# Kernel tuning notes

Measured on AMD Instinct MI355X. Metric: run time of the kernel, lower is better.

Reference implementation:

```python
import jax, jax.numpy as jnp
import numpy as np

D_MODEL = 1024
NUM_HEADS = 16
D_K = D_MODEL // NUM_HEADS
D_FF = 4096
EPS = 1e-5


def setup_inputs() -> dict:
    key = jax.random.key(0)
    ks = jax.random.split(key, 16)
    B, S = 2, 2048
    s_attn = 1.0 / np.sqrt(D_MODEL)
    s_ff1 = 1.0 / np.sqrt(D_MODEL)
    s_ff2 = 1.0 / np.sqrt(D_FF)
    return {
        "x": jax.random.normal(ks[0], (B, S, D_MODEL), jnp.float32),
        "Wq": jax.random.normal(ks[1], (D_MODEL, D_MODEL), jnp.float32) * s_attn,
        "bq": jnp.zeros((D_MODEL,), jnp.float32),
        "Wk": jax.random.normal(ks[2], (D_MODEL, D_MODEL), jnp.float32) * s_attn,
        "bk": jnp.zeros((D_MODEL,), jnp.float32),
        "Wv": jax.random.normal(ks[3], (D_MODEL, D_MODEL), jnp.float32) * s_attn,
        "bv": jnp.zeros((D_MODEL,), jnp.float32),
        "Wo": jax.random.normal(ks[4], (D_MODEL, D_MODEL), jnp.float32) * s_attn,
        "bo": jnp.zeros((D_MODEL,), jnp.float32),
        "W1": jax.random.normal(ks[5], (D_MODEL, D_FF), jnp.float32) * s_ff1,
        "b1": jnp.zeros((D_FF,), jnp.float32),
        "W2": jax.random.normal(ks[6], (D_FF, D_MODEL), jnp.float32) * s_ff2,
        "b2": jnp.zeros((D_MODEL,), jnp.float32),
        "g1": jnp.ones((D_MODEL,), jnp.float32),
        "be1": jnp.zeros((D_MODEL,), jnp.float32),
        "g2": jnp.ones((D_MODEL,), jnp.float32),
        "be2": jnp.zeros((D_MODEL,), jnp.float32),
    }


def _layernorm(x, g, b):
    m = jnp.mean(x, axis=-1, keepdims=True)
    v = jnp.mean(jnp.square(x - m), axis=-1, keepdims=True)
    return (x - m) * jax.lax.rsqrt(v + EPS) * g + b


def _split_heads(x, B, S):
    # (B, S, D) -> (B, H, S, d_k)
    return x.reshape(B, S, NUM_HEADS, D_K).transpose(0, 2, 1, 3)


def reference(x, Wq, bq, Wk, bk, Wv, bv, Wo, bo, W1, b1, W2, b2, g1, be1, g2, be2):
    B, S, _ = x.shape
    Q = _split_heads(x @ Wq + bq, B, S)
    K = _split_heads(x @ Wk + bk, B, S)
    V = _split_heads(x @ Wv + bv, B, S)
    scores = jnp.einsum("bhqd,bhkd->bhqk", Q, K) / np.sqrt(D_K).astype(np.float32)
    attn = jax.nn.softmax(scores, axis=-1)  # dropout is identity (p=0 / eval)
    ctx = jnp.einsum("bhqk,bhkd->bhqd", attn, V)
    ctx = ctx.transpose(0, 2, 1, 3).reshape(B, S, D_MODEL)
    attn_out = ctx @ Wo + bo
    h = _layernorm(x + attn_out, g1, be1)
    ff = jax.nn.relu(h @ W1 + b1) @ W2 + b2
    out = _layernorm(h + ff, g2, be2)
    return out, attn
```

## Files before the change

### kernel.cpp

```cpp
#include <hip/hip_runtime.h>
#include <cstddef>
#include <cstdint>

#define D_MODEL 1024
#define NUM_HEADS 16
#define DK 64
#define D_FF 4096
#define SEQ 2048
#define BATCH 2
#define EPS 1e-5f

typedef unsigned short u16;
typedef __attribute__((ext_vector_type(8))) short bf16x8;
typedef __attribute__((ext_vector_type(8))) unsigned short us8;
typedef __attribute__((ext_vector_type(4))) unsigned short us4;
typedef __attribute__((ext_vector_type(4))) float f32x4;

#define SBAR() asm volatile("s_barrier" ::: "memory")

__device__ __forceinline__ u16 f2b(float f) {
    unsigned u = __float_as_uint(f);
    u += 0x7fffu + ((u >> 16) & 1u);
    return (u16)(u >> 16);
}
__device__ __forceinline__ float b2f(u16 v) {
    return __uint_as_float((unsigned)v << 16);
}

__device__ __forceinline__ void gload16(const void* g, void* l) {
    __builtin_amdgcn_global_load_lds(
        (const __attribute__((address_space(1))) void*)g,
        (__attribute__((address_space(3))) void*)l, 16, 0, 0);
}

__device__ __forceinline__ void stage_half(
    const u16* __restrict__ g, int ld, long kbase, int h,
    u16* dst, int tid, int wid)
{
#pragma unroll
    for (int r = 0; r < 2; ++r) {
        const int ci  = r * 512 + tid;
        const int row = ci >> 2;
        const int wd  = ci & 3;
        const int f   = (row + (row >> 2)) & 3;
        const long src = (long)row * ld + kbase + (long)(h * 4 + (wd ^ f)) * 8;
        gload16(g + src, dst + (r * 512 + wid * 64) * 8);
    }
}

__device__ __forceinline__ bf16x8 frag64(const u16* base, int ks, int row, int g) {
    const int f = (row + (row >> 2)) & 3;
    return *(const bf16x8*)&base[ks * 8192 + row * 32 + ((g ^ f) * 8)];
}

template<int KTOT, bool RELU>
__global__ __launch_bounds__(512, 2) void gemm256(
    const u16* __restrict__ Abf, const u16* __restrict__ BT,
    const float* __restrict__ bias0, u16* __restrict__ C0,
    int ldc, int nx)
{
    constexpr int NT = KTOT / 64;
    __shared__ u16 lds[2][32768];

    const int tid = threadIdx.x;
    const int wid = tid >> 6, l = tid & 63;
    const int r16 = l & 15, g = l >> 4;
    const int wr = wid >> 2, wc = wid & 3;

    const int nwg = gridDim.x;
    const int q = nwg >> 3, rr = nwg & 7;
    const int xcd = blockIdx.x & 7, idx = blockIdx.x >> 3;
    const int wg = (xcd < rr ? xcd * (q + 1) : rr * (q + 1) + (xcd - rr) * q) + idx;
    const long bm = (long)(wg / nx) * 256;
    const long bn = (long)(wg % nx) * 256;

    const u16* Ag = Abf + bm * KTOT;
    const u16* Bg = BT + bn * KTOT;

    f32x4 acc[8][4];
#pragma unroll
    for (int i = 0; i < 8; ++i)
#pragma unroll
        for (int n = 0; n < 4; ++n)
            acc[i][n] = (f32x4){0.f, 0.f, 0.f, 0.f};

    stage_half(Ag, KTOT, 0, 0, &lds[0][0],     tid, wid);
    stage_half(Ag, KTOT, 0, 1, &lds[0][8192],  tid, wid);
    stage_half(Bg, KTOT, 0, 0, &lds[0][16384], tid, wid);
    stage_half(Bg, KTOT, 0, 1, &lds[0][24576], tid, wid);
    if (NT > 1) {
        stage_half(Ag, KTOT, 64, 0, &lds[1][0],     tid, wid);
        stage_half(Bg, KTOT, 64, 0, &lds[1][16384], tid, wid);
    }
    asm volatile("s_waitcnt vmcnt(4)" ::: "memory");
    SBAR();

    for (int t = 0; t < NT; ++t) {
        u16* cur = &lds[t & 1][0];
        u16* nxt = &lds[(t + 1) & 1][0];
        const long k1 = (long)(t + 1) * 64;
        const long k2 = (long)(t + 2) * 64;
        const bool s1 = (t + 1 < NT), s2 = (t + 2 < NT);

        bf16x8 a0[4], b0[4];
#pragma unroll
        for (int i = 0; i < 4; ++i) {
            a0[i] = frag64(cur,         0, wr * 128 + i * 16 + r16, g);
            b0[i] = frag64(cur + 16384, 0, wc * 64  + i * 16 + r16, g);
        }
        if (s1) stage_half(Ag, KTOT, k1, 1, nxt + 8192, tid, wid);
        SBAR();
        __builtin_amdgcn_s_setprio(1);
#pragma unroll
        for (int i = 0; i < 4; ++i)
#pragma unroll
            for (int n = 0; n < 4; ++n)
                acc[i][n] = __builtin_amdgcn_mfma_f32_16x16x32_bf16(
                    a0[i], b0[n], acc[i][n], 0, 0, 0);
        __builtin_amdgcn_s_setprio(0);
        SBAR();

        bf16x8 a1[4];
#pragma unroll
        for (int i = 0; i < 4; ++i)
            a1[i] = frag64(cur, 0, wr * 128 + (i + 4) * 16 + r16, g);
        if (s1) stage_half(Bg, KTOT, k1, 1, nxt + 24576, tid, wid);
        SBAR();
        __builtin_amdgcn_s_setprio(1);
#pragma unroll
        for (int i = 0; i < 4; ++i)
#pragma unroll
            for (int n = 0; n < 4; ++n)
                acc[i + 4][n] = __builtin_amdgcn_mfma_f32_16x16x32_bf16(
                    a1[i], b0[n], acc[i + 4][n], 0, 0, 0);
        __builtin_amdgcn_s_setprio(0);
        SBAR();

        bf16x8 a2[4], b1[4];
#pragma unroll
        for (int i = 0; i < 4; ++i) {
            a2[i] = frag64(cur,         1, wr * 128 + i * 16 + r16, g);
            b1[i] = frag64(cur + 16384, 1, wc * 64  + i * 16 + r16, g);
        }
        if (s2) stage_half(Ag, KTOT, k2, 0, cur, tid, wid);
        SBAR();
        __builtin_amdgcn_s_setprio(1);
#pragma unroll
        for (int i = 0; i < 4; ++i)
#pragma unroll
            for (int n = 0; n < 4; ++n)
                acc[i][n] = __builtin_amdgcn_mfma_f32_16x16x32_bf16(
                    a2[i], b1[n], acc[i][n], 0, 0, 0);
        __builtin_amdgcn_s_setprio(0);
        SBAR();

        bf16x8 a3[4];
#pragma unroll
        for (int i = 0; i < 4; ++i)
            a3[i] = frag64(cur, 1, wr * 128 + (i + 4) * 16 + r16, g);
        if (s2) stage_half(Bg, KTOT, k2, 0, cur + 16384, tid, wid);
        SBAR();
        __builtin_amdgcn_s_setprio(1);
#pragma unroll
        for (int i = 0; i < 4; ++i)
#pragma unroll
            for (int n = 0; n < 4; ++n)
                acc[i + 4][n] = __builtin_amdgcn_mfma_f32_16x16x32_bf16(
                    a3[i], b1[n], acc[i + 4][n], 0, 0, 0);
        __builtin_amdgcn_s_setprio(0);
        if (s2)      asm volatile("s_waitcnt vmcnt(4)" ::: "memory");
        else if (s1) asm volatile("s_waitcnt vmcnt(0)" ::: "memory");
        SBAR();
    }

    const long crow0 = bm + wr * 128 + g * 4;
    const long ccol0 = bn + wc * 64 + r16;
#pragma unroll
    for (int n = 0; n < 4; ++n) {
        const long col = ccol0 + n * 16;
        const float bv = bias0[col];
#pragma unroll
        for (int i = 0; i < 8; ++i)
#pragma unroll
            for (int j = 0; j < 4; ++j) {
                const long row = crow0 + i * 16 + j;
                float v = acc[i][n][j] + bv;
                if (RELU) v = fmaxf(v, 0.f);
                C0[row * (long)ldc + col] = f2b(v);
            }
    }
}

template<bool RELU, int NSPLIT>
__global__ __launch_bounds__(256) void gemm_mfma(
    const u16* __restrict__ Abf, const u16* __restrict__ BT,
    const float* __restrict__ bias0, const float* __restrict__ bias1,
    const float* __restrict__ bias2,
    u16* __restrict__ C0, u16* __restrict__ C1, u16* __restrict__ C2,
    int lda, int ldb, int ldc, int K, int nx)
{
    constexpr int BM = 128, BN = 128;
    constexpr int MI = 4, NI = 4;
    constexpr int RA = 2, RB = 2;
    constexpr int TILE = (BM + BN) * 32;

    __shared__ u16 sm[2][TILE];

    const int tid = threadIdx.x;
    const int w = tid >> 6, l = tid & 63;
    const int r16 = l & 15, g = l >> 4;
    const int wr = w >> 1, wc = w & 1;

    const int nwg = gridDim.x;
    const int q = nwg >> 3, rr = nwg & 7;
    const int xcd = blockIdx.x & 7, idx = blockIdx.x >> 3;
    const int wg = (xcd < rr ? xcd * (q + 1) : rr * (q + 1) + (xcd - rr) * q) + idx;
    const long bm = (long)(wg / nx) * BM;
    const long bn = (long)(wg % nx) * BN;

    f32x4 acc[MI][NI];
#pragma unroll
    for (int mi = 0; mi < MI; ++mi)
#pragma unroll
        for (int ni = 0; ni < NI; ++ni)
            acc[mi][ni] = (f32x4){0.f, 0.f, 0.f, 0.f};

    long aOff[RA], bOff[RB];
#pragma unroll
    for (int r = 0; r < RA; ++r) {
        int c = r * 256 + tid;
        aOff[r] = (long)(bm + (c >> 2)) * lda + (c & 3) * 8;
    }
#pragma unroll
    for (int r = 0; r < RB; ++r) {
        int c = r * 256 + tid;
        bOff[r] = (long)(bn + (c >> 2)) * ldb + (c & 3) * 8;
    }

#pragma unroll
    for (int r = 0; r < RA; ++r)
        gload16(Abf + aOff[r], &sm[0][0] + (r * 256 + w * 64) * 8);
#pragma unroll
    for (int r = 0; r < RB; ++r)
        gload16(BT + bOff[r], &sm[0][BM * 32] + (r * 256 + w * 64) * 8);
    __syncthreads();

    int cur = 0;
    for (int k0 = 0; k0 < K; k0 += 32) {
        if (k0 + 32 < K) {
            const int nxt = cur ^ 1;
#pragma unroll
            for (int r = 0; r < RA; ++r)
                gload16(Abf + aOff[r] + k0 + 32, &sm[nxt][0] + (r * 256 + w * 64) * 8);
#pragma unroll
            for (int r = 0; r < RB; ++r)
                gload16(BT + bOff[r] + k0 + 32, &sm[nxt][BM * 32] + (r * 256 + w * 64) * 8);
        }

        const u16* smA = &sm[cur][0];
        const u16* smB = &sm[cur][BM * 32];
        bf16x8 af[MI], bfr[NI];
#pragma unroll
        for (int mi = 0; mi < MI; ++mi)
            af[mi] = *(const bf16x8*)&smA[(wr * 64 + mi * 16 + r16) * 32 + g * 8];
#pragma unroll
        for (int ni = 0; ni < NI; ++ni)
            bfr[ni] = *(const bf16x8*)&smB[(wc * 64 + ni * 16 + r16) * 32 + g * 8];
#pragma unroll
        for (int mi = 0; mi < MI; ++mi)
#pragma unroll
            for (int ni = 0; ni < NI; ++ni)
                acc[mi][ni] = __builtin_amdgcn_mfma_f32_16x16x32_bf16(
                    af[mi], bfr[ni], acc[mi][ni], 0, 0, 0);

        __syncthreads();
        cur ^= 1;
    }

    u16* Cb = C0; const float* bp = bias0; long coff = 0;
    if (NSPLIT == 3) {
        const int grp = (int)(bn >> 10);
        if (grp == 1)      { Cb = C1; bp = bias1; }
        else if (grp == 2) { Cb = C2; bp = bias2; }
        coff = (long)grp << 10;
    }
    const long crow0 = bm + wr * 64 + g * 4;
    const long ccol0 = bn + wc * 64 + r16 - coff;
#pragma unroll
    for (int ni = 0; ni < NI; ++ni) {
        const long col = ccol0 + ni * 16;
        const float bv = bp[col];
#pragma unroll
        for (int mi = 0; mi < MI; ++mi) {
#pragma unroll
            for (int j = 0; j < 4; ++j) {
                const long row = crow0 + mi * 16 + j;
                float v = acc[mi][ni][j] + bv;
                if (RELU) v = fmaxf(v, 0.f);
                Cb[row * (long)ldc + col] = f2b(v);
            }
        }
    }
}

#define QBLK 128
#define KBLK 64
#define NTT (SEQ / KBLK)
#define C2E 0.18033688f

__global__ __launch_bounds__(256) void flash_attn(
    const u16* __restrict__ Qg, const u16* __restrict__ Kg,
    const u16* __restrict__ Vt, float* __restrict__ attn,
    u16* __restrict__ ctx)
{
    __shared__ u16 smem[16384];
    __shared__ u16 Ps[4][2048];
    __shared__ float stats[4][32];

    u16* const Qs  = smem;
    u16* const kb0 = smem + 8192;
    u16* const kb1 = smem;

    const int tid = threadIdx.x;
    const int w = tid >> 6, l = tid & 63;
    const int r16 = l & 15, g = l >> 4;

    const int wg = (blockIdx.x & 7) * (gridDim.x >> 3) + (blockIdx.x >> 3);
    const int qb = wg & 15, z = wg >> 4;
    const int b = z >> 4, h = z & 15;
    const long q0 = (long)qb * QBLK;

    const long kBase = ((long)b * SEQ) * D_MODEL + h * DK;
    const long vBase = (long)z * DK * SEQ;

#pragma unroll
    for (int r = 0; r < 4; ++r) {
        int c = r * 256 + tid;
        int row = c >> 3, bl = c & 7;
        long src = ((long)b * SEQ + q0 + row) * D_MODEL + h * DK
                 + ((bl ^ (row & 7)) * 8);
        gload16(Qg + src, Qs + (r * 256 + w * 64) * 8);
    }
#pragma unroll
    for (int r = 0; r < 2; ++r) {
        int c = r * 256 + tid;
        int row = c >> 3, bl = c & 7;
        gload16(Kg + kBase + (long)row * D_MODEL + ((bl ^ (row & 7)) * 8),
                kb0 + (r * 256 + w * 64) * 8);
    }
    __syncthreads();

    bf16x8 qf[2][2];
#pragma unroll
    for (int qi = 0; qi < 2; ++qi)
#pragma unroll
        for (int ks = 0; ks < 2; ++ks)
            qf[qi][ks] = *(const bf16x8*)
                &Qs[(w * 32 + qi * 16 + r16) * 64 + (((ks * 4 + g) ^ (r16 & 7)) * 8)];
    __syncthreads();

    float lrun[2] = {0.f, 0.f};

    for (int t = 0; t < NTT; ++t) {
        if (t + 1 < NTT) {
            u16* kdst = ((t + 1) & 1) ? kb1 : kb0;
            const long kro = (long)(t + 1) * KBLK;
#pragma unroll
            for (int r = 0; r < 2; ++r) {
                int c = r * 256 + tid;
                int row = c >> 3, bl = c & 7;
                gload16(Kg + kBase + (kro + row) * D_MODEL + ((bl ^ (row & 7)) * 8),
                        kdst + (r * 256 + w * 64) * 8);
            }
        }
        const u16* kcur = (t & 1) ? kb1 : kb0;

        f32x4 sT[4][2];
#pragma unroll
        for (int ki = 0; ki < 4; ++ki)
#pragma unroll
            for (int qi = 0; qi < 2; ++qi) sT[ki][qi] = (f32x4){0.f, 0.f, 0.f, 0.f};

        __builtin_amdgcn_s_setprio(1);
#pragma unroll
        for (int ks = 0; ks < 2; ++ks) {
            bf16x8 kf[4];
#pragma unroll
            for (int ki = 0; ki < 4; ++ki)
                kf[ki] = *(const bf16x8*)
                    &kcur[(ki * 16 + r16) * 64 + (((ks * 4 + g) ^ (r16 & 7)) * 8)];
#pragma unroll
            for (int ki = 0; ki < 4; ++ki)
#pragma unroll
                for (int qi = 0; qi < 2; ++qi)
                    sT[ki][qi] = __builtin_amdgcn_mfma_f32_16x16x32_bf16(
                        kf[ki], qf[qi][ks], sT[ki][qi], 0, 0, 0);
        }
        __builtin_amdgcn_s_setprio(0);

#pragma unroll
        for (int qi = 0; qi < 2; ++qi) {
            float ls = 0.f;
#pragma unroll
            for (int ki = 0; ki < 4; ++ki)
#pragma unroll
                for (int j = 0; j < 4; ++j)
                    ls += exp2f(sT[ki][qi][j] * C2E);
            ls += __shfl_xor(ls, 16);
            ls += __shfl_xor(ls, 32);
            lrun[qi] += ls;
        }
        __syncthreads();
    }

    u16* const p2b0 = smem + 8192;
    u16* const p2b1 = smem;
#pragma unroll
    for (int r = 0; r < 2; ++r) {
        int c = r * 256 + tid;
        int row = c >> 3, bl = c & 7;
        gload16(Kg + kBase + (long)row * D_MODEL + ((bl ^ (row & 7)) * 8),
                p2b0 + (r * 256 + w * 64) * 8);
        gload16(Vt + vBase + (long)row * SEQ + ((bl ^ (row & 7)) * 8),
                p2b0 + 4096 + (r * 256 + w * 64) * 8);
    }
    if (l < 16) {
        stats[w][r16]      = 1.0f / lrun[0];
        stats[w][16 + r16] = 1.0f / lrun[1];
    }
    __syncthreads();

    float il2[2][4];
#pragma unroll
    for (int mi = 0; mi < 2; ++mi)
#pragma unroll
        for (int j = 0; j < 4; ++j)
            il2[mi][j] = stats[w][mi * 16 + g * 4 + j];

    f32x4 acc2[2][4];
#pragma unroll
    for (int mi = 0; mi < 2; ++mi)
#pragma unroll
        for (int ni = 0; ni < 4; ++ni) acc2[mi][ni] = (f32x4){0.f, 0.f, 0.f, 0.f};

    for (int t = 0; t < NTT; ++t) {
        const int k0 = t * KBLK;
        if (t + 1 < NTT) {
            u16* dst = ((t + 1) & 1) ? p2b1 : p2b0;
            const long kro = (long)(t + 1) * KBLK;
#pragma unroll
            for (int r = 0; r < 2; ++r) {
                int c = r * 256 + tid;
                int row = c >> 3, bl = c & 7;
                gload16(Kg + kBase + (kro + row) * D_MODEL + ((bl ^ (row & 7)) * 8),
                        dst + (r * 256 + w * 64) * 8);
                gload16(Vt + vBase + (long)row * SEQ + kro + ((bl ^ (row & 7)) * 8),
                        dst + 4096 + (r * 256 + w * 64) * 8);
            }
        }
        const u16* kcur = (t & 1) ? p2b1 : p2b0;
        const u16* vcur = kcur + 4096;

        f32x4 s[2][4];
#pragma unroll
        for (int mi = 0; mi < 2; ++mi)
#pragma unroll
            for (int ni = 0; ni < 4; ++ni) s[mi][ni] = (f32x4){0.f, 0.f, 0.f, 0.f};

        __builtin_amdgcn_s_setprio(1);
#pragma unroll
        for (int ks = 0; ks < 2; ++ks) {
            bf16x8 kf[4];
#pragma unroll
            for (int ni = 0; ni < 4; ++ni)
                kf[ni] = *(const bf16x8*)
                    &kcur[(ni * 16 + r16) * 64 + (((ks * 4 + g) ^ (r16 & 7)) * 8)];
#pragma unroll
            for (int mi = 0; mi < 2; ++mi)
#pragma unroll
                for (int ni = 0; ni < 4; ++ni)
                    s[mi][ni] = __builtin_amdgcn_mfma_f32_16x16x32_bf16(
                        qf[mi][ks], kf[ni], s[mi][ni], 0, 0, 0);
        }
        __builtin_amdgcn_s_setprio(0);

#pragma unroll
        for (int mi = 0; mi < 2; ++mi)
#pragma unroll
            for (int j = 0; j < 4; ++j) {
                const int pr = mi * 16 + g * 4 + j;
                const long grow = (long)z * SEQ + q0 + w * 32 + pr;
#pragma unroll
                for (int ni = 0; ni < 4; ++ni) {
                    float p = exp2f(s[mi][ni][j] * C2E) * il2[mi][j];
                    const int pc = ni * 16 + r16;
                    __builtin_nontemporal_store(p, &attn[grow * SEQ + k0 + pc]);
                    Ps[w][pr * 64 + (pc ^ ((pr & 7) << 3))] = f2b(p);
                }
            }

        __builtin_amdgcn_s_setprio(1);
#pragma unroll
        for (int ks = 0; ks < 2; ++ks) {
            bf16x8 pf[2], vf[4];
#pragma unroll
            for (int mi = 0; mi < 2; ++mi)
                pf[mi] = *(const bf16x8*)
                    &Ps[w][(mi * 16 + r16) * 64 + (((ks * 4 + g) ^ (r16 & 7)) * 8)];
#pragma unroll
            for (int ni = 0; ni < 4; ++ni)
                vf[ni] = *(const bf16x8*)
                    &vcur[(ni * 16 + r16) * 64 + (((ks * 4 + g) ^ (r16 & 7)) * 8)];
#pragma unroll
            for (int mi = 0; mi < 2; ++mi)
#pragma unroll
                for (int ni = 0; ni < 4; ++ni)
                    acc2[mi][ni] = __builtin_amdgcn_mfma_f32_16x16x32_bf16(
                        pf[mi], vf[ni], acc2[mi][ni], 0, 0, 0);
        }
        __builtin_amdgcn_s_setprio(0);
        __syncthreads();
    }

#pragma unroll
    for (int mi = 0; mi < 2; ++mi)
#pragma unroll
        for (int j = 0; j < 4; ++j) {
            const long grow = (long)b * SEQ + q0 + w * 32 + mi * 16 + g * 4 + j;
#pragma unroll
            for (int ni = 0; ni < 4; ++ni)
                ctx[grow * D_MODEL + h * DK + ni * 16 + r16] = f2b(acc2[mi][ni][j]);
        }
}

__device__ __forceinline__ void tr32(
    const float* __restrict__ W, u16* __restrict__ Wt, int R, int C,
    int bx, int by, int tx, int ty, float (*t)[33])
{
    const long c = (long)bx * 32 + tx;
    const long r0 = (long)by * 32;
#pragma unroll
    for (int j = 0; j < 32; j += 8)
        t[ty + j][tx] = W[(r0 + ty + j) * C + c];
    __syncthreads();
    const long r = r0 + tx;
#pragma unroll
    for (int j = 0; j < 32; j += 8)
        Wt[((long)bx * 32 + ty + j) * R + r] = f2b(t[tx][ty + j]);
}

__global__ __launch_bounds__(256) void preproc(
    const float* __restrict__ x, u16* __restrict__ x_bf,
    const float* __restrict__ Wq, const float* __restrict__ Wk,
    const float* __restrict__ Wv, const float* __restrict__ Wo,
    u16* __restrict__ Wqkvo_t,
    const float* __restrict__ W1, u16* __restrict__ W1t,
    const float* __restrict__ W2, u16* __restrict__ W2t)
{
    __shared__ float t[32][33];
    int bid = blockIdx.x;
    const int tx = threadIdx.x & 31, ty = threadIdx.x >> 5;

    if (bid < 2048) {
        long i = ((long)bid * 256 + threadIdx.x) * 8;
        float4 a = *(const float4*)(x + i);
        float4 b = *(const float4*)(x + i + 4);
        us8 o;
        o[0] = f2b(a.x); o[1] = f2b(a.y); o[2] = f2b(a.z); o[3] = f2b(a.w);
        o[4] = f2b(b.x); o[5] = f2b(b.y); o[6] = f2b(b.z); o[7] = f2b(b.w);
        *(us8*)(x_bf + i) = o;
        return;
    }
    bid -= 2048;
    if (bid < 4096) {
        const int z = bid >> 10, rem = bid & 1023;
        const float* W = (z == 0) ? Wq : (z == 1) ? Wk : (z == 2) ? Wv : Wo;
        tr32(W, Wqkvo_t + (size_t)z * D_MODEL * D_MODEL, D_MODEL, D_MODEL,
             rem & 31, rem >> 5, tx, ty, t);
        return;
    }
    bid -= 4096;
    if (bid < 4096) {
        tr32(W1, W1t, D_MODEL, D_FF, bid & 127, bid >> 7, tx, ty, t);
        return;
    }
    bid -= 4096;
    {
        tr32(W2, W2t, D_FF, D_MODEL, bid & 31, bid >> 5, tx, ty, t);
    }
}

__global__ __launch_bounds__(256) void transpose_v(
    const u16* __restrict__ V, u16* __restrict__ Vt)
{
    __shared__ u16 t[32][33];
    const int z = blockIdx.z, b = z >> 4, h = z & 15;
    const int tx = threadIdx.x & 31, ty = threadIdx.x >> 5;
    const long k0 = (long)blockIdx.x * 32;
    const long d0 = (long)blockIdx.y * 32;
#pragma unroll
    for (int j = 0; j < 32; j += 8)
        t[ty + j][tx] = V[((long)b * SEQ + k0 + ty + j) * D_MODEL + h * DK + d0 + tx];
    __syncthreads();
#pragma unroll
    for (int j = 0; j < 32; j += 8)
        Vt[((long)z * DK + d0 + ty + j) * SEQ + k0 + tx] = t[tx][ty + j];
}

template<int OM>
__global__ __launch_bounds__(256) void add_ln_kernel(
    const u16* __restrict__ a, const u16* __restrict__ b,
    const float* __restrict__ g, const float* __restrict__ be,
    void* __restrict__ outp)
{
    const int l = threadIdx.x & 63, w = threadIdx.x >> 6;
    const long row = (long)blockIdx.x * 4 + w;
    const long base = row * D_MODEL;

    float xv[16];
#pragma unroll
    for (int c = 0; c < 2; ++c) {
        const long off = c * 512 + l * 8;
        us8 av = *(const us8*)(a + base + off);
        us8 bv = *(const us8*)(b + base + off);
#pragma unroll
        for (int i = 0; i < 8; ++i)
            xv[c * 8 + i] = b2f(av[i]) + b2f(bv[i]);
    }

    float s = 0.f;
#pragma unroll
    for (int i = 0; i < 16; ++i) s += xv[i];
#pragma unroll
    for (int off = 1; off < 64; off <<= 1) s += __shfl_xor(s, off);
    const float mean = s * (1.0f / D_MODEL);

    float ss = 0.f;
#pragma unroll
    for (int i = 0; i < 16; ++i) {
        xv[i] -= mean;
        ss += xv[i] * xv[i];
    }
#pragma unroll
    for (int off = 1; off < 64; off <<= 1) ss += __shfl_xor(ss, off);
    const float rs = rsqrtf(ss * (1.0f / D_MODEL) + EPS);

#pragma unroll
    for (int c = 0; c < 2; ++c) {
        const long off = c * 512 + l * 8;
        float4 g0 = *(const float4*)(g + off);
        float4 g1 = *(const float4*)(g + off + 4);
        float4 b0 = *(const float4*)(be + off);
        float4 b1 = *(const float4*)(be + off + 4);
        float o[8];
        o[0] = xv[c*8+0] * rs * g0.x + b0.x;
        o[1] = xv[c*8+1] * rs * g0.y + b0.y;
        o[2] = xv[c*8+2] * rs * g0.z + b0.z;
        o[3] = xv[c*8+3] * rs * g0.w + b0.w;
        o[4] = xv[c*8+4] * rs * g1.x + b1.x;
        o[5] = xv[c*8+5] * rs * g1.y + b1.y;
        o[6] = xv[c*8+6] * rs * g1.z + b1.z;
        o[7] = xv[c*8+7] * rs * g1.w + b1.w;
        if (OM == 0) {
            float4 v0 = {o[0], o[1], o[2], o[3]};
            float4 v1 = {o[4], o[5], o[6], o[7]};
            *(float4*)((float*)outp + base + off) = v0;
            *(float4*)((float*)outp + base + off + 4) = v1;
        } else {
            us8 ob;
#pragma unroll
            for (int i = 0; i < 8; ++i) ob[i] = f2b(o[i]);
            *(us8*)((u16*)outp + base + off) = ob;
        }
    }
}

extern "C" void kernel_launch(void* const* d_in, const int* in_sizes, int n_in,
                              void* d_out, int out_size, void* d_ws, size_t ws_size,
                              hipStream_t stream)
{
    const float* x   = (const float*)d_in[0];
    const float* Wq  = (const float*)d_in[1];
    const float* bq  = (const float*)d_in[2];
    const float* Wk  = (const float*)d_in[3];
    const float* bk  = (const float*)d_in[4];
    const float* Wv  = (const float*)d_in[5];
    const float* bv  = (const float*)d_in[6];
    const float* Wo  = (const float*)d_in[7];
    const float* bo  = (const float*)d_in[8];
    const float* W1  = (const float*)d_in[9];
    const float* b1  = (const float*)d_in[10];
    const float* W2  = (const float*)d_in[11];
    const float* b2  = (const float*)d_in[12];
    const float* g1  = (const float*)d_in[13];
    const float* be1 = (const float*)d_in[14];
    const float* g2  = (const float*)d_in[15];
    const float* be2 = (const float*)d_in[16];

    float* out  = (float*)d_out;
    float* attn = out + (size_t)BATCH * SEQ * D_MODEL;

    char* ws = (char*)d_ws;
    const size_t MB = 1u << 20;
    u16* x_bf    = (u16*)(ws);
    u16* Q_bf    = (u16*)(ws + 8 * MB);
    u16* K_bf    = (u16*)(ws + 16 * MB);
    u16* V_bf    = (u16*)(ws + 24 * MB);
    u16* Vt      = (u16*)(ws + 32 * MB);
    u16* Wqkvo_t = (u16*)(ws + 40 * MB);
    u16* W1t     = (u16*)(ws + 48 * MB);
    u16* W2t     = (u16*)(ws + 56 * MB);
    u16* ff1_bf  = (u16*)(ws + 64 * MB);
    u16* ctx_bf  = (u16*)(ws + 96 * MB);
    u16* Wot     = Wqkvo_t + (size_t)3 * D_MODEL * D_MODEL;
    u16* h_bf    = K_bf;
    u16* ao_bf   = V_bf;
    u16* ff2_bf  = Vt;

    const int M = BATCH * SEQ;
    dim3 T(256);

    preproc<<<dim3(2048 + 3 * 4096), T, 0, stream>>>(
        x, x_bf, Wq, Wk, Wv, Wo, Wqkvo_t, W1, W1t, W2, W2t);

    gemm_mfma<false, 3><<<dim3((M / 128) * 24), T, 0, stream>>>(
        x_bf, Wqkvo_t, bq, bk, bv, Q_bf, K_bf, V_bf,
        D_MODEL, D_MODEL, D_MODEL, D_MODEL, 24);

    transpose_v<<<dim3(SEQ / 32, DK / 32, BATCH * NUM_HEADS), T, 0, stream>>>(V_bf, Vt);

    flash_attn<<<dim3((SEQ / QBLK) * BATCH * NUM_HEADS), T, 0, stream>>>(
        Q_bf, K_bf, Vt, attn, ctx_bf);

    gemm_mfma<false, 1><<<dim3((M / 128) * 8), T, 0, stream>>>(
        ctx_bf, Wot, bo, nullptr, nullptr, ao_bf, nullptr, nullptr,
        D_MODEL, D_MODEL, D_MODEL, D_MODEL, 8);

    add_ln_kernel<1><<<dim3(M / 4), T, 0, stream>>>(x_bf, ao_bf, g1, be1, h_bf);

    gemm256<D_MODEL, true><<<dim3((M / 256) * (D_FF / 256)), dim3(512), 0, stream>>>(
        h_bf, W1t, b1, ff1_bf, D_FF, D_FF / 256);

    gemm_mfma<false, 1><<<dim3((M / 128) * 8), T, 0, stream>>>(
        ff1_bf, W2t, b2, nullptr, nullptr, ff2_bf, nullptr, nullptr,
        D_FF, D_FF, D_MODEL, D_FF, 8);

    add_ln_kernel<0><<<dim3(M / 4), T, 0, stream>>>(h_bf, ff2_bf, g2, be2, out);
}
```

Measured before the change: 409.2 us.

## Fuse V transpose into QKV GEMM epilogue and transpose scores for vector attn stores

The QKV GEMM epilogue now writes the V third directly in head-transposed layout (Vt), which removes the separate transpose_v kernel and its round trip through global memory. In the second attention pass, scores are computed as K·Q^T so each lane holds four consecutive key columns. That lets the fp32 attention probabilities go out as 16-byte nontemporal stores and the bf16 P tile be written as 8-byte LDS stores, and the per-row inverse sums now live in registers instead of a shared stats array. The V epilogue writes become 8-byte scattered stores into rows of length SEQ, which may be less coalesced than the original row-major writes.

```diff
diff --git a/kernel.cpp b/kernel.cpp
--- a/kernel.cpp
+++ b/kernel.cpp
@@ -277,14 +277,36 @@
         cur ^= 1;
     }
 
+    const long crow0 = bm + wr * 64 + g * 4;
+
+    if (NSPLIT == 3 && bn >= 2048) {
+        const int btok = (int)(crow0 >> 11);
+        const int kr0  = (int)(crow0 & 2047);
+        const long ccolV = bn + wc * 64 + r16 - 2048;
+#pragma unroll
+        for (int ni = 0; ni < NI; ++ni) {
+            const long col = ccolV + ni * 16;
+            const int h = (int)(col >> 6), d = (int)(col & 63);
+            const float bv = bias2[col];
+            const long vrow = ((long)(btok * 16 + h) * 64 + d) * (long)SEQ;
+#pragma unroll
+            for (int mi = 0; mi < MI; ++mi) {
+                us4 pv;
+#pragma unroll
+                for (int j = 0; j < 4; ++j)
+                    pv[j] = f2b(acc[mi][ni][j] + bv);
+                *(us4*)&C2[vrow + kr0 + mi * 16] = pv;
+            }
+        }
+        return;
+    }
+
     u16* Cb = C0; const float* bp = bias0; long coff = 0;
     if (NSPLIT == 3) {
         const int grp = (int)(bn >> 10);
-        if (grp == 1)      { Cb = C1; bp = bias1; }
-        else if (grp == 2) { Cb = C2; bp = bias2; }
+        if (grp == 1) { Cb = C1; bp = bias1; }
         coff = (long)grp << 10;
     }
-    const long crow0 = bm + wr * 64 + g * 4;
     const long ccol0 = bn + wc * 64 + r16 - coff;
 #pragma unroll
     for (int ni = 0; ni < NI; ++ni) {
@@ -315,7 +337,6 @@
 {
     __shared__ u16 smem[16384];
     __shared__ u16 Ps[4][2048];
-    __shared__ float stats[4][32];
 
     u16* const Qs  = smem;
     u16* const kb0 = smem + 8192;
@@ -412,6 +433,8 @@
         }
         __syncthreads();
     }
+
+    const float il[2] = {1.0f / lrun[0], 1.0f / lrun[1]};
 
     u16* const p2b0 = smem + 8192;
     u16* const p2b1 = smem;
@@ -424,24 +447,15 @@
         gload16(Vt + vBase + (long)row * SEQ + ((bl ^ (row & 7)) * 8),
                 p2b0 + 4096 + (r * 256 + w * 64) * 8);
     }
-    if (l < 16) {
-        stats[w][r16]      = 1.0f / lrun[0];
-        stats[w][16 + r16] = 1.0f / lrun[1];
-    }
     __syncthreads();
 
-    float il2[2][4];
+    f32x4 acc2[2][4];
 #pragma unroll
     for (int mi = 0; mi < 2; ++mi)
 #pragma unroll
-        for (int j = 0; j < 4; ++j)
-            il2[mi][j] = stats[w][mi * 16 + g * 4 + j];
-
-    f32x4 acc2[2][4];
-#pragma unroll
-    for (int mi = 0; mi < 2; ++mi)
-#pragma unroll
         for (int ni = 0; ni < 4; ++ni) acc2[mi][ni] = (f32x4){0.f, 0.f, 0.f, 0.f};
+
+    const long arow0 = ((long)z * SEQ + q0 + w * 32) * (long)SEQ;
 
     for (int t = 0; t < NTT; ++t) {
         const int k0 = t * KBLK;
@@ -461,43 +475,48 @@
         const u16* kcur = (t & 1) ? p2b1 : p2b0;
         const u16* vcur = kcur + 4096;
 
-        f32x4 s[2][4];
-#pragma unroll
-        for (int mi = 0; mi < 2; ++mi)
-#pragma unroll
-            for (int ni = 0; ni < 4; ++ni) s[mi][ni] = (f32x4){0.f, 0.f, 0.f, 0.f};
+        f32x4 sT[4][2];
+#pragma unroll
+        for (int ki = 0; ki < 4; ++ki)
+#pragma unroll
+            for (int qi = 0; qi < 2; ++qi) sT[ki][qi] = (f32x4){0.f, 0.f, 0.f, 0.f};
 
         __builtin_amdgcn_s_setprio(1);
 #pragma unroll
         for (int ks = 0; ks < 2; ++ks) {
             bf16x8 kf[4];
 #pragma unroll
-            for (int ni = 0; ni < 4; ++ni)
-                kf[ni] = *(const bf16x8*)
-                    &kcur[(ni * 16 + r16) * 64 + (((ks * 4 + g) ^ (r16 & 7)) * 8)];
-#pragma unroll
-            for (int mi = 0; mi < 2; ++mi)
-#pragma unroll
-                for (int ni = 0; ni < 4; ++ni)
-                    s[mi][ni] = __builtin_amdgcn_mfma_f32_16x16x32_bf16(
-                        qf[mi][ks], kf[ni], s[mi][ni], 0, 0, 0);
+            for (int ki = 0; ki < 4; ++ki)
+                kf[ki] = *(const bf16x8*)
+                    &kcur[(ki * 16 + r16) * 64 + (((ks * 4 + g) ^ (r16 & 7)) * 8)];
+#pragma unroll
+            for (int ki = 0; ki < 4; ++ki)
+#pragma unroll
+                for (int qi = 0; qi < 2; ++qi)
+                    sT[ki][qi] = __builtin_amdgcn_mfma_f32_16x16x32_bf16(
+                        kf[ki], qf[qi][ks], sT[ki][qi], 0, 0, 0);
         }
         __builtin_amdgcn_s_setprio(0);
 
 #pragma unroll
-        for (int mi = 0; mi < 2; ++mi)
-#pragma unroll
-            for (int j = 0; j < 4; ++j) {
-                const int pr = mi * 16 + g * 4 + j;
-                const long grow = (long)z * SEQ + q0 + w * 32 + pr;
-#pragma unroll
-                for (int ni = 0; ni < 4; ++ni) {
-                    float p = exp2f(s[mi][ni][j] * C2E) * il2[mi][j];
-                    const int pc = ni * 16 + r16;
-                    __builtin_nontemporal_store(p, &attn[grow * SEQ + k0 + pc]);
-                    Ps[w][pr * 64 + (pc ^ ((pr & 7) << 3))] = f2b(p);
-                }
+        for (int qi = 0; qi < 2; ++qi) {
+            const long ar = arow0 + (long)(qi * 16 + r16) * SEQ + k0 + g * 4;
+            const int prow = (qi * 16 + r16) * 64;
+#pragma unroll
+            for (int ki = 0; ki < 4; ++ki) {
+                f32x4 p;
+                p[0] = exp2f(sT[ki][qi][0] * C2E) * il[qi];
+                p[1] = exp2f(sT[ki][qi][1] * C2E) * il[qi];
+                p[2] = exp2f(sT[ki][qi][2] * C2E) * il[qi];
+                p[3] = exp2f(sT[ki][qi][3] * C2E) * il[qi];
+                __builtin_nontemporal_store(p, (f32x4*)&attn[ar + ki * 16]);
+                us4 pb;
+                pb[0] = f2b(p[0]); pb[1] = f2b(p[1]);
+                pb[2] = f2b(p[2]); pb[3] = f2b(p[3]);
+                const int kblk = 2 * ki + (g >> 1);
+                *(us4*)&Ps[w][prow + ((kblk ^ (r16 & 7)) << 3) + ((g & 1) << 2)] = pb;
             }
+        }
 
         __builtin_amdgcn_s_setprio(1);
 #pragma unroll
@@ -506,7 +525,7 @@
 #pragma unroll
             for (int mi = 0; mi < 2; ++mi)
                 pf[mi] = *(const bf16x8*)
-                    &Ps[w][(mi * 16 + r16) * 64 + (((ks * 4 + g) ^ (r16 & 7)) * 8)];
+                    &Ps[w][(mi * 16 + r16) * 64 + (((ks * 4 + g) ^ (r16 & 7)) << 3)];
 #pragma unroll
             for (int ni = 0; ni < 4; ++ni)
                 vf[ni] = *(const bf16x8*)
@@ -588,23 +607,6 @@
     {
         tr32(W2, W2t, D_FF, D_MODEL, bid & 31, bid >> 5, tx, ty, t);
     }
-}
-
-__global__ __launch_bounds__(256) void transpose_v(
-    const u16* __restrict__ V, u16* __restrict__ Vt)
-{
-    __shared__ u16 t[32][33];
-    const int z = blockIdx.z, b = z >> 4, h = z & 15;
-    const int tx = threadIdx.x & 31, ty = threadIdx.x >> 5;
-    const long k0 = (long)blockIdx.x * 32;
-    const long d0 = (long)blockIdx.y * 32;
-#pragma unroll
-    for (int j = 0; j < 32; j += 8)
-        t[ty + j][tx] = V[((long)b * SEQ + k0 + ty + j) * D_MODEL + h * DK + d0 + tx];
-    __syncthreads();
-#pragma unroll
-    for (int j = 0; j < 32; j += 8)
-        Vt[((long)z * DK + d0 + ty + j) * SEQ + k0 + tx] = t[tx][ty + j];
 }
 
 template<int OM>
@@ -705,8 +707,8 @@
     u16* x_bf    = (u16*)(ws);
     u16* Q_bf    = (u16*)(ws + 8 * MB);
     u16* K_bf    = (u16*)(ws + 16 * MB);
-    u16* V_bf    = (u16*)(ws + 24 * MB);
-    u16* Vt      = (u16*)(ws + 32 * MB);
+    u16* Vt      = (u16*)(ws + 24 * MB);
+    u16* spare   = (u16*)(ws + 32 * MB);
     u16* Wqkvo_t = (u16*)(ws + 40 * MB);
     u16* W1t     = (u16*)(ws + 48 * MB);
     u16* W2t     = (u16*)(ws + 56 * MB);
@@ -714,7 +716,7 @@
     u16* ctx_bf  = (u16*)(ws + 96 * MB);
     u16* Wot     = Wqkvo_t + (size_t)3 * D_MODEL * D_MODEL;
     u16* h_bf    = K_bf;
-    u16* ao_bf   = V_bf;
+    u16* ao_bf   = spare;
     u16* ff2_bf  = Vt;
 
     const int M = BATCH * SEQ;
@@ -724,10 +726,8 @@
         x, x_bf, Wq, Wk, Wv, Wo, Wqkvo_t, W1, W1t, W2, W2t);
 
     gemm_mfma<false, 3><<<dim3((M / 128) * 24), T, 0, stream>>>(
-        x_bf, Wqkvo_t, bq, bk, bv, Q_bf, K_bf, V_bf,
+        x_bf, Wqkvo_t, bq, bk, bv, Q_bf, K_bf, Vt,
         D_MODEL, D_MODEL, D_MODEL, D_MODEL, 24);
-
-    transpose_v<<<dim3(SEQ / 32, DK / 32, BATCH * NUM_HEADS), T, 0, stream>>>(V_bf, Vt);
 
     flash_attn<<<dim3((SEQ / QBLK) * BATCH * NUM_HEADS), T, 0, stream>>>(
         Q_bf, K_bf, Vt, attn, ctx_bf);
```

After: 424.8 us. 1.04x slower.
